# Kernel optimization log

Hardware: AMD Instinct MI355X
Metric: run time of the kernel (lower is better)

The kernel has to match this reference:

```python
import jax, jax.numpy as jnp
import numpy as np

DEPTH_PARAM = 0.5
LENGTH_PENALTY = 1.5
LEVEL_COUNTS = [8, 32, 128, 512, 2048]  # nodes per tree level (branching factor 4)
BRANCH = 4
B = 4096


def _build_tree():
    counts = LEVEL_COUNTS
    D = len(counts)
    offsets = np.concatenate([[0], np.cumsum(counts)]).astype(np.int64)
    C = int(offsets[-1])
    path_ids = np.zeros((C, D), np.int32)   # ancestor matrix-id at each level (0-padded)
    path_len = np.zeros((C,), np.int32)     # depth of this class (= len of its path)
    sib_start = np.zeros((C, D), np.int32)  # start of contiguous sibling block at each level
    sib_size = np.zeros((C, D), np.int32)   # size of that block (valid_classes in torch code)
    for l in range(D):
        for k in range(counts[l]):
            gid = offsets[l] + k
            path_len[gid] = l + 1
            kk = k
            for a in range(l, -1, -1):
                path_ids[gid, a] = offsets[a] + kk
                if a == 0:
                    sib_start[gid, a] = 0
                    sib_size[gid, a] = counts[0]
                else:
                    sib_start[gid, a] = offsets[a] + (kk // BRANCH) * BRANCH
                    sib_size[gid, a] = BRANCH
                kk = kk // BRANCH
    return path_ids, path_len, sib_start, sib_size, C


def setup_inputs() -> dict:
    path_ids, path_len, sib_start, sib_size, C = _build_tree()
    key = jax.random.key(0)
    k1, k2 = jax.random.split(key)
    y_pred = jax.random.normal(k1, (B, C), dtype=jnp.float32)
    y_true = jax.random.normal(k2, (B, C), dtype=jnp.float32)  # only argmax is used
    rng = np.random.default_rng(0)
    counts = rng.integers(1, 1000, size=C).astype(np.float32)
    class_weights = jnp.asarray(counts.max() / counts, dtype=jnp.float32)
    return {
        "y_pred": y_pred,
        "y_true": y_true,
        "class_weights": class_weights,
        "path_ids": jnp.asarray(path_ids),
        "path_len": jnp.asarray(path_len),
        "sib_start": jnp.asarray(sib_start),
        "sib_size": jnp.asarray(sib_size),
    }


def reference(y_pred, y_true, class_weights, path_ids, path_len, sib_start, sib_size):
    Bsz, C = y_pred.shape
    D = path_ids.shape[1]
    pred_top = jnp.argmax(y_pred, axis=1)                    # [B]
    true_top = jnp.argmax(y_true, axis=1)                    # [B]
    len_p = path_len[pred_top]                               # [B]
    len_t = path_len[true_top]                               # [B]
    levels = jnp.arange(D)                                   # [D]
    # level in range(min(len(pred_path), len(true_path)))
    valid = levels[None, :] < jnp.minimum(len_p, len_t)[:, None]        # [B,D]
    height = (len_t[:, None] - levels[None, :] - 1).astype(y_pred.dtype)
    level_w = jnp.exp(-DEPTH_PARAM * height)                            # [B,D]
    t_ids = path_ids[true_top]                                          # [B,D]
    start = sib_start[true_top]                                         # [B,D]
    stop = start + sib_size[true_top]                                   # [B,D]
    cls = jnp.arange(C)
    mask = ((cls[None, None, :] >= start[:, :, None]) &
            (cls[None, None, :] < stop[:, :, None])).astype(y_pred.dtype)  # [B,D,C]
    # torch code multiplies logits by the 0/1 mask (NOT -inf masking)
    logits = y_pred[:, None, :] * mask                                  # [B,D,C]
    lse = jax.nn.logsumexp(logits, axis=-1)                             # [B,D]
    true_logit = jnp.take_along_axis(logits, t_ids[:, :, None], axis=-1)[..., 0]
    ce = lse - true_logit                                               # per-level cross entropy
    local = jnp.sum(jnp.where(valid, level_w * ce, 0.0), axis=1)        # [B]
    diff = jnp.abs(len_p - len_t).astype(y_pred.dtype)
    total = local * (LENGTH_PENALTY * diff) * class_weights[true_top]
    return jnp.mean(total)
```

## Files before the change

kernel.cpp:

```cpp
#include <hip/hip_runtime.h>
#include <hip/hip_bf16.h>
#include <float.h>

#define DEPTH_PARAM 0.5f
#define LENGTH_PENALTY 1.5f

__global__ __launch_bounds__(256) void hier_row_kernel(
    const float* __restrict__ y_pred,
    const float* __restrict__ y_true,
    const float* __restrict__ class_weights,
    const int* __restrict__ path_ids,
    const int* __restrict__ path_len,
    const int* __restrict__ sib_start,
    const int* __restrict__ sib_size,
    float* __restrict__ row_total,
    int C, int D, int Bsz)
{
    const int wid  = threadIdx.x >> 6;
    const int lane = threadIdx.x & 63;
    const int half = wid & 1;
    int row = blockIdx.x * 2 + (wid >> 1);
    if (row >= Bsz) row = Bsz - 1;

    const float* __restrict__ yp = y_pred + (size_t)row * C;
    const float* __restrict__ yt = y_true + (size_t)row * C;

    float bp = -FLT_MAX; int bip = 0;
    float bt = -FLT_MAX; int bit_ = 0;
    const int C4 = C >> 2;
    const float4* __restrict__ yp4 = (const float4*)yp;
    const float4* __restrict__ yt4 = (const float4*)yt;

    for (int i = half * 64 + lane; i < C4; i += 128) {
        float4 v = yp4[i];
        float4 w = yt4[i];
        int base = i << 2;
        if (v.x > bp) { bp = v.x; bip = base + 0; }
        if (v.y > bp) { bp = v.y; bip = base + 1; }
        if (v.z > bp) { bp = v.z; bip = base + 2; }
        if (v.w > bp) { bp = v.w; bip = base + 3; }
        if (w.x > bt) { bt = w.x; bit_ = base + 0; }
        if (w.y > bt) { bt = w.y; bit_ = base + 1; }
        if (w.z > bt) { bt = w.z; bit_ = base + 2; }
        if (w.w > bt) { bt = w.w; bit_ = base + 3; }
    }
    for (int c = (C4 << 2) + half * 64 + lane; c < C; c += 128) {
        float v = yp[c]; if (v > bp) { bp = v; bip = c; }
        float w = yt[c]; if (w > bt) { bt = w; bit_ = c; }
    }

    for (int m = 1; m < 64; m <<= 1) {
        float ov = __shfl_xor(bp, m); int oi = __shfl_xor(bip, m);
        if (ov > bp || (ov == bp && oi < bip)) { bp = ov; bip = oi; }
        float ow = __shfl_xor(bt, m); int oj = __shfl_xor(bit_, m);
        if (ow > bt || (ow == bt && oj < bit_)) { bt = ow; bit_ = oj; }
    }

    __shared__ float s_v[4][2];
    __shared__ int   s_i[4][2];
    if (lane == 0) {
        s_v[wid][0] = bp;  s_i[wid][0] = bip;
        s_v[wid][1] = bt;  s_i[wid][1] = bit_;
    }
    __syncthreads();
    {
        const int pw = wid ^ 1;
        float ov = s_v[pw][0]; int oi = s_i[pw][0];
        if (ov > bp || (ov == bp && oi < bip)) { bp = ov; bip = oi; }
        float ow = s_v[pw][1]; int oj = s_i[pw][1];
        if (ow > bt || (ow == bt && oj < bit_)) { bt = ow; bit_ = oj; }
    }

    if (half == 0) {
        const int pred_top = bip;
        const int true_top = bit_;
        const int lp = path_len[pred_top];
        const int lt = path_len[true_top];
        const int lmin = lp < lt ? lp : lt;

        const int l = lane >> 3;
        const int j = lane & 7;
        float contrib = 0.0f;
        float e = 0.0f;
        int st = 0, sz = 0;
        if (l < lmin) {
            st = sib_start[true_top * D + l];
            sz = sib_size[true_top * D + l];
            if (j < sz) e = expf(yp[st + j]);
        }
        e += __shfl_xor(e, 1);
        e += __shfl_xor(e, 2);
        e += __shfl_xor(e, 4);
        if (l < lmin && j == 0) {
            const float s = e + (float)(C - sz);
            const int tix = path_ids[true_top * D + l];
            const float ce = logf(s) - yp[tix];
            const float lw = expf(-DEPTH_PARAM * (float)(lt - l - 1));
            contrib = lw * ce;
        }
        contrib += __shfl_xor(contrib, 8);
        contrib += __shfl_xor(contrib, 16);
        contrib += __shfl_xor(contrib, 32);

        if (lane == 0) {
            const float diff = fabsf((float)(lp - lt));
            row_total[row] = contrib * (LENGTH_PENALTY * diff) * class_weights[true_top];
        }
    }
}

__global__ __launch_bounds__(256) void final_reduce_kernel(
    const float* __restrict__ row_total, float* __restrict__ out, int Bsz)
{
    const int tid = threadIdx.x;
    float s = 0.0f;
    for (int i = tid; i < Bsz; i += 256) s += row_total[i];
    for (int m = 1; m < 64; m <<= 1) s += __shfl_xor(s, m);

    __shared__ float sw[4];
    const int lane = tid & 63, wid = tid >> 6;
    if (lane == 0) sw[wid] = s;
    __syncthreads();
    if (tid == 0) {
        float t = sw[0] + sw[1] + sw[2] + sw[3];
        out[0] = t / (float)Bsz;
    }
}

extern "C" void kernel_launch(void* const* d_in, const int* in_sizes, int n_in,
                              void* d_out, int out_size, void* d_ws, size_t ws_size,
                              hipStream_t stream) {
    const float* y_pred        = (const float*)d_in[0];
    const float* y_true        = (const float*)d_in[1];
    const float* class_weights = (const float*)d_in[2];
    const int*   path_ids      = (const int*)d_in[3];
    const int*   path_len      = (const int*)d_in[4];
    const int*   sib_start     = (const int*)d_in[5];
    const int*   sib_size      = (const int*)d_in[6];
    float* out = (float*)d_out;
    float* row_total = (float*)d_ws;

    const int C = in_sizes[2];
    const int D = in_sizes[3] / C;
    const int B = in_sizes[0] / C;

    const int grid = (B + 1) / 2;
    hier_row_kernel<<<grid, 256, 0, stream>>>(
        y_pred, y_true, class_weights, path_ids, path_len,
        sib_start, sib_size, row_total, C, D, B);
    final_reduce_kernel<<<1, 256, 0, stream>>>(row_total, out, B);
}
```

Baseline: 120.2 us.

## Specialize row kernel on compile-time C and fold final reduce into atomics

Adds a templated row kernel for C=2728 that issues all float4 loads up front into register arrays before the argmax scan, so more memory requests are in flight per lane. The separate final-reduce kernel is replaced by a per-row atomicAdd into the output, which a tiny init kernel zeroes first. This trades one serial reduction launch for an init launch plus contended atomics. Float summation order becomes nondeterministic.

```diff
diff --git a/kernel.cpp b/kernel.cpp
--- a/kernel.cpp
+++ b/kernel.cpp
@@ -5,7 +5,10 @@
 #define DEPTH_PARAM 0.5f
 #define LENGTH_PENALTY 1.5f
 
-__global__ __launch_bounds__(256) void hier_row_kernel(
+__global__ void init_out_kernel(float* out) { out[0] = 0.0f; }
+
+template<int C>
+__global__ __launch_bounds__(256) void hier_row_kernel_t(
     const float* __restrict__ y_pred,
     const float* __restrict__ y_true,
     const float* __restrict__ class_weights,
@@ -13,24 +16,148 @@
     const int* __restrict__ path_len,
     const int* __restrict__ sib_start,
     const int* __restrict__ sib_size,
-    float* __restrict__ row_total,
+    float* __restrict__ out,
+    int D, int Bsz)
+{
+    constexpr int C4  = C >> 2;
+    constexpr int NIT = (C4 + 127) / 128;
+
+    const int wid  = threadIdx.x >> 6;
+    const int lane = threadIdx.x & 63;
+    const int half = wid & 1;
+    int row = blockIdx.x * 2 + (wid >> 1);
+    bool edge_dup = false;
+    if (row >= Bsz) { row = Bsz - 1; edge_dup = true; }
+
+    const float* __restrict__ yp = y_pred + (size_t)row * C;
+    const float* __restrict__ yt = y_true + (size_t)row * C;
+    const float4* __restrict__ yp4 = (const float4*)yp;
+    const float4* __restrict__ yt4 = (const float4*)yt;
+
+    float4 vv[NIT], ww[NIT];
+    const int i0 = half * 64 + lane;
+#pragma unroll
+    for (int k = 0; k < NIT; k++) {
+        const int i = i0 + k * 128;
+        if (i < C4) {
+            vv[k] = yp4[i];
+            ww[k] = yt4[i];
+        } else {
+            vv[k] = make_float4(-FLT_MAX, -FLT_MAX, -FLT_MAX, -FLT_MAX);
+            ww[k] = make_float4(-FLT_MAX, -FLT_MAX, -FLT_MAX, -FLT_MAX);
+        }
+    }
+
+    float bp = -FLT_MAX; int bip = 0;
+    float bt = -FLT_MAX; int bit_ = 0;
+#pragma unroll
+    for (int k = 0; k < NIT; k++) {
+        const int base = (i0 + k * 128) << 2;
+        const float4 v = vv[k];
+        const float4 w = ww[k];
+        if (v.x > bp) { bp = v.x; bip = base + 0; }
+        if (v.y > bp) { bp = v.y; bip = base + 1; }
+        if (v.z > bp) { bp = v.z; bip = base + 2; }
+        if (v.w > bp) { bp = v.w; bip = base + 3; }
+        if (w.x > bt) { bt = w.x; bit_ = base + 0; }
+        if (w.y > bt) { bt = w.y; bit_ = base + 1; }
+        if (w.z > bt) { bt = w.z; bit_ = base + 2; }
+        if (w.w > bt) { bt = w.w; bit_ = base + 3; }
+    }
+    if constexpr ((C & 3) != 0) {
+        for (int c = (C4 << 2) + half * 64 + lane; c < C; c += 128) {
+            float v = yp[c]; if (v > bp) { bp = v; bip = c; }
+            float w = yt[c]; if (w > bt) { bt = w; bit_ = c; }
+        }
+    }
+
+    for (int m = 1; m < 64; m <<= 1) {
+        float ov = __shfl_xor(bp, m); int oi = __shfl_xor(bip, m);
+        if (ov > bp || (ov == bp && oi < bip)) { bp = ov; bip = oi; }
+        float ow = __shfl_xor(bt, m); int oj = __shfl_xor(bit_, m);
+        if (ow > bt || (ow == bt && oj < bit_)) { bt = ow; bit_ = oj; }
+    }
+
+    __shared__ float s_v[4][2];
+    __shared__ int   s_i[4][2];
+    if (lane == 0) {
+        s_v[wid][0] = bp;  s_i[wid][0] = bip;
+        s_v[wid][1] = bt;  s_i[wid][1] = bit_;
+    }
+    __syncthreads();
+    {
+        const int pw = wid ^ 1;
+        float ov = s_v[pw][0]; int oi = s_i[pw][0];
+        if (ov > bp || (ov == bp && oi < bip)) { bp = ov; bip = oi; }
+        float ow = s_v[pw][1]; int oj = s_i[pw][1];
+        if (ow > bt || (ow == bt && oj < bit_)) { bt = ow; bit_ = oj; }
+    }
+
+    if (half == 0 && !edge_dup) {
+        const int pred_top = bip;
+        const int true_top = bit_;
+        const int lp = path_len[pred_top];
+        const int lt = path_len[true_top];
+        const int lmin = lp < lt ? lp : lt;
+
+        const int l = lane >> 3;
+        const int j = lane & 7;
+        float e = 0.0f;
+        int sz = 0;
+        if (l < lmin) {
+            const int st = sib_start[true_top * D + l];
+            sz = sib_size[true_top * D + l];
+            if (j < sz) e = expf(yp[st + j]);
+        }
+        e += __shfl_xor(e, 1);
+        e += __shfl_xor(e, 2);
+        e += __shfl_xor(e, 4);
+        float contrib = 0.0f;
+        if (l < lmin && j == 0) {
+            const float s = e + (float)(C - sz);
+            const int tix = path_ids[true_top * D + l];
+            const float ce = logf(s) - yp[tix];
+            const float lw = expf(-DEPTH_PARAM * (float)(lt - l - 1));
+            contrib = lw * ce;
+        }
+        contrib += __shfl_xor(contrib, 8);
+        contrib += __shfl_xor(contrib, 16);
+        contrib += __shfl_xor(contrib, 32);
+
+        if (lane == 0) {
+            const float diff = fabsf((float)(lp - lt));
+            const float total = contrib * (LENGTH_PENALTY * diff) * class_weights[true_top];
+            atomicAdd(out, total / (float)Bsz);
+        }
+    }
+}
+
+__global__ __launch_bounds__(256) void hier_row_kernel_g(
+    const float* __restrict__ y_pred,
+    const float* __restrict__ y_true,
+    const float* __restrict__ class_weights,
+    const int* __restrict__ path_ids,
+    const int* __restrict__ path_len,
+    const int* __restrict__ sib_start,
+    const int* __restrict__ sib_size,
+    float* __restrict__ out,
     int C, int D, int Bsz)
 {
     const int wid  = threadIdx.x >> 6;
     const int lane = threadIdx.x & 63;
     const int half = wid & 1;
     int row = blockIdx.x * 2 + (wid >> 1);
-    if (row >= Bsz) row = Bsz - 1;
+    bool edge_dup = false;
+    if (row >= Bsz) { row = Bsz - 1; edge_dup = true; }
 
     const float* __restrict__ yp = y_pred + (size_t)row * C;
     const float* __restrict__ yt = y_true + (size_t)row * C;
+    const float4* __restrict__ yp4 = (const float4*)yp;
+    const float4* __restrict__ yt4 = (const float4*)yt;
 
     float bp = -FLT_MAX; int bip = 0;
     float bt = -FLT_MAX; int bit_ = 0;
     const int C4 = C >> 2;
-    const float4* __restrict__ yp4 = (const float4*)yp;
-    const float4* __restrict__ yt4 = (const float4*)yt;
-
     for (int i = half * 64 + lane; i < C4; i += 128) {
         float4 v = yp4[i];
         float4 w = yt4[i];
@@ -48,14 +175,12 @@
         float v = yp[c]; if (v > bp) { bp = v; bip = c; }
         float w = yt[c]; if (w > bt) { bt = w; bit_ = c; }
     }
-
     for (int m = 1; m < 64; m <<= 1) {
         float ov = __shfl_xor(bp, m); int oi = __shfl_xor(bip, m);
         if (ov > bp || (ov == bp && oi < bip)) { bp = ov; bip = oi; }
         float ow = __shfl_xor(bt, m); int oj = __shfl_xor(bit_, m);
         if (ow > bt || (ow == bt && oj < bit_)) { bt = ow; bit_ = oj; }
     }
-
     __shared__ float s_v[4][2];
     __shared__ int   s_i[4][2];
     if (lane == 0) {
@@ -70,27 +195,25 @@
         float ow = s_v[pw][1]; int oj = s_i[pw][1];
         if (ow > bt || (ow == bt && oj < bit_)) { bt = ow; bit_ = oj; }
     }
-
-    if (half == 0) {
+    if (half == 0 && !edge_dup) {
         const int pred_top = bip;
         const int true_top = bit_;
         const int lp = path_len[pred_top];
         const int lt = path_len[true_top];
         const int lmin = lp < lt ? lp : lt;
-
         const int l = lane >> 3;
         const int j = lane & 7;
-        float contrib = 0.0f;
         float e = 0.0f;
-        int st = 0, sz = 0;
+        int sz = 0;
         if (l < lmin) {
-            st = sib_start[true_top * D + l];
+            const int st = sib_start[true_top * D + l];
             sz = sib_size[true_top * D + l];
             if (j < sz) e = expf(yp[st + j]);
         }
         e += __shfl_xor(e, 1);
         e += __shfl_xor(e, 2);
         e += __shfl_xor(e, 4);
+        float contrib = 0.0f;
         if (l < lmin && j == 0) {
             const float s = e + (float)(C - sz);
             const int tix = path_ids[true_top * D + l];
@@ -101,29 +224,11 @@
         contrib += __shfl_xor(contrib, 8);
         contrib += __shfl_xor(contrib, 16);
         contrib += __shfl_xor(contrib, 32);
-
         if (lane == 0) {
             const float diff = fabsf((float)(lp - lt));
-            row_total[row] = contrib * (LENGTH_PENALTY * diff) * class_weights[true_top];
-        }
-    }
-}
-
-__global__ __launch_bounds__(256) void final_reduce_kernel(
-    const float* __restrict__ row_total, float* __restrict__ out, int Bsz)
-{
-    const int tid = threadIdx.x;
-    float s = 0.0f;
-    for (int i = tid; i < Bsz; i += 256) s += row_total[i];
-    for (int m = 1; m < 64; m <<= 1) s += __shfl_xor(s, m);
-
-    __shared__ float sw[4];
-    const int lane = tid & 63, wid = tid >> 6;
-    if (lane == 0) sw[wid] = s;
-    __syncthreads();
-    if (tid == 0) {
-        float t = sw[0] + sw[1] + sw[2] + sw[3];
-        out[0] = t / (float)Bsz;
+            const float total = contrib * (LENGTH_PENALTY * diff) * class_weights[true_top];
+            atomicAdd(out, total / (float)Bsz);
+        }
     }
 }
 
@@ -138,15 +243,20 @@
     const int*   sib_start     = (const int*)d_in[5];
     const int*   sib_size      = (const int*)d_in[6];
     float* out = (float*)d_out;
-    float* row_total = (float*)d_ws;
 
     const int C = in_sizes[2];
     const int D = in_sizes[3] / C;
     const int B = in_sizes[0] / C;
 
     const int grid = (B + 1) / 2;
-    hier_row_kernel<<<grid, 256, 0, stream>>>(
-        y_pred, y_true, class_weights, path_ids, path_len,
-        sib_start, sib_size, row_total, C, D, B);
-    final_reduce_kernel<<<1, 256, 0, stream>>>(row_total, out, B);
+    init_out_kernel<<<1, 1, 0, stream>>>(out);
+    if (C == 2728) {
+        hier_row_kernel_t<2728><<<grid, 256, 0, stream>>>(
+            y_pred, y_true, class_weights, path_ids, path_len,
+            sib_start, sib_size, out, D, B);
+    } else {
+        hier_row_kernel_g<<<grid, 256, 0, stream>>>(
+            y_pred, y_true, class_weights, path_ids, path_len,
+            sib_start, sib_size, out, C, D, B);
+    }
 }
```

Result: slower. 164.5 us (+36.8%).

## Split argmax per wave by tensor and fuse final mean via atomics

Applied to the files above, without the earlier changes.

Each row's two waves now scan whole rows of y_pred and y_true separately, instead of both interleaving over the two tensors. Only the indices are exchanged through shared memory. The separate final reduction kernel and workspace array are replaced by a per-row atomicAdd into the output, which a tiny init kernel zeroes first. This removes one reduction pass and simplifies the inner loop, but adds 4096 atomics onto a single address, makes the summation order nondeterministic, and adds a kernel launch.

```diff
diff --git a/kernel.cpp b/kernel.cpp
--- a/kernel.cpp
+++ b/kernel.cpp
@@ -4,6 +4,8 @@
 
 #define DEPTH_PARAM 0.5f
 #define LENGTH_PENALTY 1.5f
+
+__global__ void init_out_kernel(float* out) { out[0] = 0.0f; }
 
 __global__ __launch_bounds__(256) void hier_row_kernel(
     const float* __restrict__ y_pred,
@@ -13,84 +15,67 @@
     const int* __restrict__ path_len,
     const int* __restrict__ sib_start,
     const int* __restrict__ sib_size,
-    float* __restrict__ row_total,
+    float* __restrict__ out,
     int C, int D, int Bsz)
 {
-    const int wid  = threadIdx.x >> 6;
-    const int lane = threadIdx.x & 63;
-    const int half = wid & 1;
+    const int wid     = threadIdx.x >> 6;
+    const int lane    = threadIdx.x & 63;
+    const int is_true = wid & 1;
     int row = blockIdx.x * 2 + (wid >> 1);
-    if (row >= Bsz) row = Bsz - 1;
+    bool edge_dup = false;
+    if (row >= Bsz) { row = Bsz - 1; edge_dup = true; }
 
-    const float* __restrict__ yp = y_pred + (size_t)row * C;
-    const float* __restrict__ yt = y_true + (size_t)row * C;
+    const float* __restrict__ src =
+        (is_true ? y_true : y_pred) + (size_t)row * C;
+    const float4* __restrict__ src4 = (const float4*)src;
+    const int C4 = C >> 2;
 
-    float bp = -FLT_MAX; int bip = 0;
-    float bt = -FLT_MAX; int bit_ = 0;
-    const int C4 = C >> 2;
-    const float4* __restrict__ yp4 = (const float4*)yp;
-    const float4* __restrict__ yt4 = (const float4*)yt;
-
-    for (int i = half * 64 + lane; i < C4; i += 128) {
-        float4 v = yp4[i];
-        float4 w = yt4[i];
-        int base = i << 2;
-        if (v.x > bp) { bp = v.x; bip = base + 0; }
-        if (v.y > bp) { bp = v.y; bip = base + 1; }
-        if (v.z > bp) { bp = v.z; bip = base + 2; }
-        if (v.w > bp) { bp = v.w; bip = base + 3; }
-        if (w.x > bt) { bt = w.x; bit_ = base + 0; }
-        if (w.y > bt) { bt = w.y; bit_ = base + 1; }
-        if (w.z > bt) { bt = w.z; bit_ = base + 2; }
-        if (w.w > bt) { bt = w.w; bit_ = base + 3; }
+    float bv = -FLT_MAX; int bi = 0;
+    for (int i = lane; i < C4; i += 64) {
+        const float4 v = src4[i];
+        const int base = i << 2;
+        if (v.x > bv) { bv = v.x; bi = base + 0; }
+        if (v.y > bv) { bv = v.y; bi = base + 1; }
+        if (v.z > bv) { bv = v.z; bi = base + 2; }
+        if (v.w > bv) { bv = v.w; bi = base + 3; }
     }
-    for (int c = (C4 << 2) + half * 64 + lane; c < C; c += 128) {
-        float v = yp[c]; if (v > bp) { bp = v; bip = c; }
-        float w = yt[c]; if (w > bt) { bt = w; bit_ = c; }
+    for (int c = (C4 << 2) + lane; c < C; c += 64) {
+        const float v = src[c];
+        if (v > bv) { bv = v; bi = c; }
     }
 
     for (int m = 1; m < 64; m <<= 1) {
-        float ov = __shfl_xor(bp, m); int oi = __shfl_xor(bip, m);
-        if (ov > bp || (ov == bp && oi < bip)) { bp = ov; bip = oi; }
-        float ow = __shfl_xor(bt, m); int oj = __shfl_xor(bit_, m);
-        if (ow > bt || (ow == bt && oj < bit_)) { bt = ow; bit_ = oj; }
+        const float ov = __shfl_xor(bv, m);
+        const int   oi = __shfl_xor(bi, m);
+        if (ov > bv || (ov == bv && oi < bi)) { bv = ov; bi = oi; }
     }
 
-    __shared__ float s_v[4][2];
-    __shared__ int   s_i[4][2];
-    if (lane == 0) {
-        s_v[wid][0] = bp;  s_i[wid][0] = bip;
-        s_v[wid][1] = bt;  s_i[wid][1] = bit_;
-    }
+    __shared__ int s_idx[4];
+    if (lane == 0) s_idx[wid] = bi;
     __syncthreads();
-    {
-        const int pw = wid ^ 1;
-        float ov = s_v[pw][0]; int oi = s_i[pw][0];
-        if (ov > bp || (ov == bp && oi < bip)) { bp = ov; bip = oi; }
-        float ow = s_v[pw][1]; int oj = s_i[pw][1];
-        if (ow > bt || (ow == bt && oj < bit_)) { bt = ow; bit_ = oj; }
-    }
 
-    if (half == 0) {
-        const int pred_top = bip;
-        const int true_top = bit_;
+    if (is_true == 0 && !edge_dup) {
+        const int pred_top = bi;
+        const int true_top = s_idx[wid | 1];
         const int lp = path_len[pred_top];
         const int lt = path_len[true_top];
         const int lmin = lp < lt ? lp : lt;
 
+        const float* __restrict__ yp = y_pred + (size_t)row * C;
+
         const int l = lane >> 3;
         const int j = lane & 7;
-        float contrib = 0.0f;
         float e = 0.0f;
-        int st = 0, sz = 0;
+        int sz = 0;
         if (l < lmin) {
-            st = sib_start[true_top * D + l];
+            const int st = sib_start[true_top * D + l];
             sz = sib_size[true_top * D + l];
             if (j < sz) e = expf(yp[st + j]);
         }
         e += __shfl_xor(e, 1);
         e += __shfl_xor(e, 2);
         e += __shfl_xor(e, 4);
+        float contrib = 0.0f;
         if (l < lmin && j == 0) {
             const float s = e + (float)(C - sz);
             const int tix = path_ids[true_top * D + l];
@@ -104,26 +89,9 @@
 
         if (lane == 0) {
             const float diff = fabsf((float)(lp - lt));
-            row_total[row] = contrib * (LENGTH_PENALTY * diff) * class_weights[true_top];
+            const float total = contrib * (LENGTH_PENALTY * diff) * class_weights[true_top];
+            atomicAdd(out, total / (float)Bsz);
         }
-    }
-}
-
-__global__ __launch_bounds__(256) void final_reduce_kernel(
-    const float* __restrict__ row_total, float* __restrict__ out, int Bsz)
-{
-    const int tid = threadIdx.x;
-    float s = 0.0f;
-    for (int i = tid; i < Bsz; i += 256) s += row_total[i];
-    for (int m = 1; m < 64; m <<= 1) s += __shfl_xor(s, m);
-
-    __shared__ float sw[4];
-    const int lane = tid & 63, wid = tid >> 6;
-    if (lane == 0) sw[wid] = s;
-    __syncthreads();
-    if (tid == 0) {
-        float t = sw[0] + sw[1] + sw[2] + sw[3];
-        out[0] = t / (float)Bsz;
     }
 }
 
@@ -138,15 +106,14 @@
     const int*   sib_start     = (const int*)d_in[5];
     const int*   sib_size      = (const int*)d_in[6];
     float* out = (float*)d_out;
-    float* row_total = (float*)d_ws;
 
     const int C = in_sizes[2];
     const int D = in_sizes[3] / C;
     const int B = in_sizes[0] / C;
 
     const int grid = (B + 1) / 2;
+    init_out_kernel<<<1, 1, 0, stream>>>(out);
     hier_row_kernel<<<grid, 256, 0, stream>>>(
         y_pred, y_true, class_weights, path_ids, path_len,
-        sib_start, sib_size, row_total, C, D, B);
-    final_reduce_kernel<<<1, 256, 0, stream>>>(row_total, out, B);
+        sib_start, sib_size, out, C, D, B);
 }
```

After: 167.5 us. 1.39x slower.
